# Performance work log

Hardware: AMD Instinct MI355X
Metric: run time of the kernel (lower is better)

The kernel has to match this reference:

```python
import jax, jax.numpy as jnp
import numpy as np

NUM_BOND_TYPE = 6
NUM_BOND_DIRECTION = 3
HIDDEN = 128
OUT = 128


def setup_inputs() -> dict:
    key = jax.random.key(0)
    ks = jax.random.split(key, 12)
    N, E = 50000, 800000
    x = jax.random.normal(ks[0], (N, HIDDEN), dtype=jnp.float32)
    edge_index = jax.random.randint(ks[1], (2, E), 0, N, dtype=jnp.int64 if jax.config.jax_enable_x64 else jnp.int32)
    edge_attr = jax.random.randint(ks[2], (E, 2), 0, 3, dtype=edge_index.dtype)
    mask_node_indices = jax.random.randint(ks[3], (5000,), 0, N, dtype=edge_index.dtype)
    s = 1.0 / np.sqrt(HIDDEN)
    W_enc = jax.random.uniform(ks[4], (HIDDEN, HIDDEN), jnp.float32, -s, s)  # enc_to_dec, no bias
    W1 = jax.random.uniform(ks[5], (2 * HIDDEN, HIDDEN), jnp.float32, -s, s)
    b1 = jax.random.uniform(ks[6], (2 * HIDDEN,), jnp.float32, -s, s)
    s2 = 1.0 / np.sqrt(2 * HIDDEN)
    W2 = jax.random.uniform(ks[7], (OUT, 2 * HIDDEN), jnp.float32, -s2, s2)
    b2 = jax.random.uniform(ks[8], (OUT,), jnp.float32, -s2, s2)
    # xavier_uniform for embeddings
    g1 = np.sqrt(6.0 / (NUM_BOND_TYPE + HIDDEN))
    g2 = np.sqrt(6.0 / (NUM_BOND_DIRECTION + HIDDEN))
    emb1 = jax.random.uniform(ks[9], (NUM_BOND_TYPE, HIDDEN), jnp.float32, -g1, g1)
    emb2 = jax.random.uniform(ks[10], (NUM_BOND_DIRECTION, HIDDEN), jnp.float32, -g2, g2)
    prelu_a = jnp.array(0.25, dtype=jnp.float32)
    return {"x": x, "edge_index": edge_index, "edge_attr": edge_attr,
            "mask_node_indices": mask_node_indices, "prelu_a": prelu_a,
            "W_enc": W_enc, "W1": W1, "b1": b1, "W2": W2, "b2": b2,
            "emb1": emb1, "emb2": emb2}


def reference(x, edge_index, edge_attr, mask_node_indices, prelu_a,
              W_enc, W1, b1, W2, b2, emb1, emb2):
    N = x.shape[0]
    # PReLU activation then enc_to_dec linear (no bias)
    h = jnp.where(x > 0, x, prelu_a * x)
    h = h @ W_enc.T
    # zero out masked nodes
    h = h.at[mask_node_indices].set(0.0)
    # add self loops
    loops = jnp.arange(N, dtype=edge_index.dtype)
    src = jnp.concatenate([edge_index[0], loops])
    dst = jnp.concatenate([edge_index[1], loops])
    # self-loop edge_attr: [4, 0]
    sl_attr = jnp.concatenate([jnp.full((N, 1), 4, dtype=edge_attr.dtype),
                               jnp.zeros((N, 1), dtype=edge_attr.dtype)], axis=1)
    ea = jnp.concatenate([edge_attr, sl_attr], axis=0)
    edge_emb = emb1[ea[:, 0]] + emb2[ea[:, 1]]  # [E+N, H]
    # message: x_j + edge_attr, aggregate (add) at target nodes
    msg = h[src] + edge_emb
    aggr = jax.ops.segment_sum(msg, dst, num_segments=N)  # [N, H]
    # GIN update MLP: H -> 2H -> OUT
    out = jax.nn.relu(aggr @ W1.T + b1) @ W2.T + b2
    return out
```

## Files before the change

kernel.cpp:

```cpp
#include <hip/hip_runtime.h>

#define HID 128
#define HID2 256
#define NBMAX 3200
#define STRIDE 384

typedef __attribute__((ext_vector_type(8))) short bf16x8;
typedef __attribute__((ext_vector_type(4))) float f32x4;

__device__ inline ushort f2b(float f) {
    union { float f; unsigned u; } v; v.f = f;
    unsigned r = v.u + 0x7FFF + ((v.u >> 16) & 1);
    return (ushort)(r >> 16);
}
__device__ inline float b2f(unsigned hi16) {
    union { unsigned u; float f; } v; v.u = hi16 << 16;
    return v.f;
}

#define SZ0 (HID * HID)
#define SZ1 (HID2 * HID)
#define SZ2 (HID * HID2)

__global__ __launch_bounds__(256) void k_prep(const float* __restrict__ w0,
                                              const float* __restrict__ w1,
                                              const float* __restrict__ w2,
                                              const float* __restrict__ e1,
                                              const float* __restrict__ e2,
                                              ushort* __restrict__ o0,
                                              ushort* __restrict__ o1,
                                              ushort* __restrict__ o2,
                                              ushort* __restrict__ comboT,
                                              int* __restrict__ gcursor) {
    int i = blockIdx.x * 256 + threadIdx.x;
    if (i < SZ0) { o0[i] = f2b(w0[i]); return; }
    i -= SZ0;
    if (i < SZ1) { o1[i] = f2b(w1[i]); return; }
    i -= SZ1;
    if (i < SZ2) { o2[i] = f2b(w2[i]); return; }
    i -= SZ2;
    if (i < 4096) {
        int col = i >> 5, tt = i & 31;
        float v = 0.f;
        if (tt < 18) v = e1[(tt / 3) * HID + col] + e2[(tt % 3) * HID + col];
        comboT[col * 32 + tt] = f2b(v);
        return;
    }
    i -= 4096;
    if (i < 4096) gcursor[i] = i * STRIDE;
}

__global__ __launch_bounds__(256) void k_prelu(const float* __restrict__ x,
                                               const float* __restrict__ pa,
                                               ushort* __restrict__ p, int total8) {
    int i = blockIdx.x * 256 + threadIdx.x;
    if (i >= total8) return;
    const float a = pa[0];
    float4 v0 = *(const float4*)(x + (size_t)i * 8);
    float4 v1 = *(const float4*)(x + (size_t)i * 8 + 4);
    float vv[8] = {v0.x, v0.y, v0.z, v0.w, v1.x, v1.y, v1.z, v1.w};
    ushort u[8];
#pragma unroll
    for (int j = 0; j < 8; ++j) {
        float f = vv[j] > 0.f ? vv[j] : a * vv[j];
        u[j] = f2b(f);
    }
    *(bf16x8*)(p + (size_t)i * 8) = *(bf16x8*)u;
}

__global__ void k_mask(const int* __restrict__ idx, ushort* __restrict__ p) {
    *(unsigned*)(p + (size_t)idx[blockIdx.x] * HID + 2 * threadIdx.x) = 0u;
}

__global__ __launch_bounds__(256) void k_bscat(const int* __restrict__ src,
                                               const int* __restrict__ dst,
                                               const int* __restrict__ ea,
                                               int* __restrict__ gcursor,
                                               unsigned* __restrict__ bucketed,
                                               int E, int nbuck) {
    __shared__ int lh[NBMAX];
    __shared__ int gbs[NBMAX];
    const int t = threadIdx.x;
    const int base = blockIdx.x * 4096;
    for (int i = t; i < nbuck; i += 256) lh[i] = 0;
    __syncthreads();
    unsigned keys[16];
    int bk[16];
    int rk[16];
#pragma unroll
    for (int j = 0; j < 16; ++j) {
        int e = base + j * 256 + t;
        bk[j] = -1;
        if (e < E) {
            int d = dst[e];
            int cm = ea[2 * e] * 3 + ea[2 * e + 1];
            keys[j] = (unsigned)src[e] | ((unsigned)(d & 15) << 16) | ((unsigned)cm << 20);
            bk[j] = d >> 4;
            rk[j] = atomicAdd(&lh[bk[j]], 1);
        }
    }
    __syncthreads();
    for (int i = t; i < nbuck; i += 256) gbs[i] = lh[i] ? atomicAdd(&gcursor[i], lh[i]) : 0;
    __syncthreads();
#pragma unroll
    for (int j = 0; j < 16; ++j)
        if (bk[j] >= 0) {
            int pos = gbs[bk[j]] + rk[j];
            int lim = (bk[j] + 1) * STRIDE;
            if (pos < lim) bucketed[pos] = keys[j];
        }
}

__global__ __launch_bounds__(512) void k_baccum3(const ushort* __restrict__ p,
                                                 const int* __restrict__ gcursor,
                                                 const unsigned* __restrict__ bucketed,
                                                 ushort* __restrict__ A,
                                                 ushort* __restrict__ A2, int N) {
    __shared__ unsigned skeys[STRIDE];
    __shared__ int cnt[16];
    __shared__ int soff[16];
    __shared__ int cur[16];
    __shared__ int cnts[16][18];
    const int t = threadIdx.x;
    const int n0 = blockIdx.x << 4;
    const int w = t >> 6, l = t & 63;
    const int g = l >> 4, c16 = l & 15;

    for (int i = t; i < 16 * 18; i += 512) cnts[i / 18][i % 18] = ((i % 18) == 12) ? 1 : 0;

    float acc[2][8];
#pragma unroll
    for (int nn = 0; nn < 2; ++nn) {
        int gn = n0 + w * 2 + nn;
        uint4 pv = {0u, 0u, 0u, 0u};
        if (g == 0 && gn < N) pv = *(const uint4*)(p + (size_t)gn * HID + c16 * 8);
#pragma unroll
        for (int q = 0; q < 4; ++q) {
            unsigned u = (&pv.x)[q];
            acc[nn][2 * q]     = (g == 0) ? b2f(u & 0xffffu) : 0.f;
            acc[nn][2 * q + 1] = (g == 0) ? b2f(u >> 16) : 0.f;
        }
    }

    const int s0 = blockIdx.x * STRIDE;
    const int m = gcursor[blockIdx.x] - s0;
    if (t < 16) cnt[t] = 0;
    __syncthreads();
    if (t < m) atomicAdd(&cnt[(bucketed[s0 + t] >> 16) & 15], 1);
    __syncthreads();
    if (t < 16) {
        int v = cnt[t];
        int sc = v;
#pragma unroll
        for (int o = 1; o < 16; o <<= 1) {
            int u = __shfl_up(sc, o, 64);
            if (t >= o) sc += u;
        }
        soff[t] = sc - v;
        cur[t] = sc - v;
    }
    __syncthreads();
    if (t < m) {
        unsigned key = bucketed[s0 + t];
        int dl = (key >> 16) & 15;
        int r = atomicAdd(&cur[dl], 1);
        skeys[r] = key;
        atomicAdd(&cnts[dl][key >> 20], 1);
    }
    __syncthreads();
#pragma unroll
    for (int nn = 0; nn < 2; ++nn) {
        const int node = w * 2 + nn;
        const int eb = soff[node];
        const int c = cnt[node];
        for (int k = 0; k < c; k += 16) {
            int iA = k + g, iB = k + 4 + g, iC = k + 8 + g, iD = k + 12 + g;
            bool vA = iA < c, vB = iB < c, vC = iC < c, vD = iD < c;
            unsigned keyA = skeys[eb + (vA ? iA : c - 1)];
            unsigned keyB = skeys[eb + (vB ? iB : c - 1)];
            unsigned keyC = skeys[eb + (vC ? iC : c - 1)];
            unsigned keyD = skeys[eb + (vD ? iD : c - 1)];
            uint4 pa4 = *(const uint4*)(p + (size_t)(keyA & 0xffffu) * HID + c16 * 8);
            uint4 pb4 = *(const uint4*)(p + (size_t)(keyB & 0xffffu) * HID + c16 * 8);
            uint4 pc4 = *(const uint4*)(p + (size_t)(keyC & 0xffffu) * HID + c16 * 8);
            uint4 pd4 = *(const uint4*)(p + (size_t)(keyD & 0xffffu) * HID + c16 * 8);
#pragma unroll
            for (int q = 0; q < 4; ++q) {
                unsigned ua = (&pa4.x)[q], ub = (&pb4.x)[q];
                unsigned uc = (&pc4.x)[q], ud = (&pd4.x)[q];
                float s0f = (vA ? b2f(ua & 0xffffu) : 0.f) + (vB ? b2f(ub & 0xffffu) : 0.f)
                          + (vC ? b2f(uc & 0xffffu) : 0.f) + (vD ? b2f(ud & 0xffffu) : 0.f);
                float s1f = (vA ? b2f(ua >> 16) : 0.f) + (vB ? b2f(ub >> 16) : 0.f)
                          + (vC ? b2f(uc >> 16) : 0.f) + (vD ? b2f(ud >> 16) : 0.f);
                acc[nn][2 * q]     += s0f;
                acc[nn][2 * q + 1] += s1f;
            }
        }
    }
#pragma unroll
    for (int nn = 0; nn < 2; ++nn) {
        int gn = n0 + w * 2 + nn;
        unsigned ou[4];
#pragma unroll
        for (int q = 0; q < 4; ++q) {
            float v0 = acc[nn][2 * q], v1 = acc[nn][2 * q + 1];
            v0 += __shfl_xor(v0, 16, 64); v1 += __shfl_xor(v1, 16, 64);
            v0 += __shfl_xor(v0, 32, 64); v1 += __shfl_xor(v1, 32, 64);
            ou[q] = (unsigned)f2b(v0) | ((unsigned)f2b(v1) << 16);
        }
        if (g == 0 && gn < N)
            *(uint4*)(A + (size_t)gn * HID + c16 * 8) = *(uint4*)ou;
    }
    __syncthreads();
    if (t < 16 * 16) {
        int r = t >> 4, cp = t & 15;
        int gn = n0 + r;
        if (gn < N) {
            int i0 = 2 * cp, i1 = 2 * cp + 1;
            ushort u0 = (i0 < 18) ? f2b((float)cnts[r][i0]) : (ushort)0;
            ushort u1 = (i1 < 18) ? f2b((float)cnts[r][i1]) : (ushort)0;
            *(unsigned*)(A2 + (size_t)gn * 32 + 2 * cp) = (unsigned)u0 | ((unsigned)u1 << 16);
        }
    }
}

__global__ __launch_bounds__(256) void k_fused(const ushort* __restrict__ A,
                                               const ushort* __restrict__ A2,
                                               const ushort* __restrict__ Wencb,
                                               const ushort* __restrict__ comboT,
                                               const ushort* __restrict__ W1b,
                                               const float* __restrict__ b1,
                                               const ushort* __restrict__ W2b,
                                               const float* __restrict__ b2,
                                               float* __restrict__ out, int N) {
    __shared__ char smem[53248];
    const int t = threadIdx.x;
    const int bn = blockIdx.x * 64;
    {
        int seg = t & 15, r0 = t >> 4;
#pragma unroll
        for (int i = 0; i < 4; ++i) {
            int row = r0 + i * 16;
            int grow = bn + row;
            bf16x8 v;
            if (grow < N) v = *(const bf16x8*)(A + (size_t)grow * HID + seg * 8);
            else { ushort z[8] = {0,0,0,0,0,0,0,0}; v = *(bf16x8*)z; }
            *(bf16x8*)(smem + row * 256 + ((seg * 16) ^ ((row & 7) << 4))) = v;
        }
    }
    {
        int row = t >> 2, seg = t & 3;
        int grow = bn + row;
        bf16x8 v;
        if (grow < N) v = *(const bf16x8*)(A2 + (size_t)grow * 32 + seg * 8);
        else { ushort z[8] = {0,0,0,0,0,0,0,0}; v = *(bf16x8*)z; }
        *(bf16x8*)(smem + 16384 + row * 64 + ((seg * 16) ^ ((row & 3) << 4))) = v;
    }
    __syncthreads();
    const int w = t >> 6, l = t & 63;
    const int lrow = l & 15, lk = l >> 4;
    {
        bf16x8 wf[2][4], cf[2];
#pragma unroll
        for (int j = 0; j < 2; ++j) {
            int n = (2 * w + j) * 16 + lrow;
#pragma unroll
            for (int ks = 0; ks < 4; ++ks)
                wf[j][ks] = *(const bf16x8*)(Wencb + n * HID + ks * 32 + lk * 8);
            cf[j] = *(const bf16x8*)(comboT + n * 32 + lk * 8);
        }
#pragma unroll
        for (int rt = 0; rt < 4; ++rt) {
            int arow = rt * 16 + lrow;
            bf16x8 af[4], a2f;
#pragma unroll
            for (int ks = 0; ks < 4; ++ks)
                af[ks] = *(const bf16x8*)(smem + arow * 256 + ((ks * 64 + lk * 16) ^ ((arow & 7) << 4)));
            a2f = *(const bf16x8*)(smem + 16384 + arow * 64 + ((lk * 16) ^ ((arow & 3) << 4)));
#pragma unroll
            for (int j = 0; j < 2; ++j) {
                f32x4 acc = {0.f, 0.f, 0.f, 0.f};
#pragma unroll
                for (int ks = 0; ks < 4; ++ks)
                    acc = __builtin_amdgcn_mfma_f32_16x16x32_bf16(af[ks], wf[j][ks], acc, 0, 0, 0);
                acc = __builtin_amdgcn_mfma_f32_16x16x32_bf16(a2f, cf[j], acc, 0, 0, 0);
                int n = (2 * w + j) * 16 + lrow;
#pragma unroll
                for (int r = 0; r < 4; ++r) {
                    int row2 = rt * 16 + lk * 4 + r;
                    *(ushort*)(smem + 20480 + row2 * 256 + ((2 * n) ^ ((row2 & 7) << 4))) = f2b(acc[r]);
                }
            }
        }
    }
    __syncthreads();
    {
        bf16x8 wf[4][4];
        float bb[4];
#pragma unroll
        for (int j = 0; j < 4; ++j) {
            int n = (4 * w + j) * 16 + lrow;
#pragma unroll
            for (int ks = 0; ks < 4; ++ks)
                wf[j][ks] = *(const bf16x8*)(W1b + n * HID + ks * 32 + lk * 8);
            bb[j] = b1[n];
        }
        const int h2base = (w < 2) ? 0 : 36864;
        const int colbase = (w < 2) ? 0 : 128;
#pragma unroll
        for (int rt = 0; rt < 4; ++rt) {
            int arow = rt * 16 + lrow;
            bf16x8 af[4];
#pragma unroll
            for (int ks = 0; ks < 4; ++ks)
                af[ks] = *(const bf16x8*)(smem + 20480 + arow * 256 + ((ks * 64 + lk * 16) ^ ((arow & 7) << 4)));
#pragma unroll
            for (int j = 0; j < 4; ++j) {
                f32x4 acc = {0.f, 0.f, 0.f, 0.f};
#pragma unroll
                for (int ks = 0; ks < 4; ++ks)
                    acc = __builtin_amdgcn_mfma_f32_16x16x32_bf16(af[ks], wf[j][ks], acc, 0, 0, 0);
                int cl = (4 * w + j) * 16 + lrow - colbase;
#pragma unroll
                for (int r = 0; r < 4; ++r) {
                    float v = acc[r] + bb[j];
                    v = v > 0.f ? v : 0.f;
                    int row2 = rt * 16 + lk * 4 + r;
                    *(ushort*)(smem + h2base + row2 * 256 + ((2 * cl) ^ ((row2 & 7) << 4))) = f2b(v);
                }
            }
        }
    }
    __syncthreads();
    {
        bf16x8 wf[2][8];
        float bb[2];
#pragma unroll
        for (int j = 0; j < 2; ++j) {
            int n = (2 * w + j) * 16 + lrow;
#pragma unroll
            for (int ks = 0; ks < 8; ++ks)
                wf[j][ks] = *(const bf16x8*)(W2b + n * HID2 + ks * 32 + lk * 8);
            bb[j] = b2[n];
        }
#pragma unroll
        for (int rt = 0; rt < 4; ++rt) {
            int arow = rt * 16 + lrow;
            bf16x8 af[8];
#pragma unroll
            for (int ks = 0; ks < 4; ++ks)
                af[ks] = *(const bf16x8*)(smem + arow * 256 + ((ks * 64 + lk * 16) ^ ((arow & 7) << 4)));
#pragma unroll
            for (int ks = 4; ks < 8; ++ks)
                af[ks] = *(const bf16x8*)(smem + 36864 + arow * 256 + (((ks - 4) * 64 + lk * 16) ^ ((arow & 7) << 4)));
#pragma unroll
            for (int j = 0; j < 2; ++j) {
                f32x4 acc = {0.f, 0.f, 0.f, 0.f};
#pragma unroll
                for (int ks = 0; ks < 8; ++ks)
                    acc = __builtin_amdgcn_mfma_f32_16x16x32_bf16(af[ks], wf[j][ks], acc, 0, 0, 0);
                int n = (2 * w + j) * 16 + lrow;
#pragma unroll
                for (int r = 0; r < 4; ++r) {
                    int grow = bn + rt * 16 + lk * 4 + r;
                    if (grow < N) out[(size_t)grow * HID + n] = acc[r] + bb[j];
                }
            }
        }
    }
}

extern "C" void kernel_launch(void* const* d_in, const int* in_sizes, int n_in,
                              void* d_out, int out_size, void* d_ws, size_t ws_size,
                              hipStream_t stream) {
    const float* x     = (const float*)d_in[0];
    const int*   eidx  = (const int*)d_in[1];
    const int*   eattr = (const int*)d_in[2];
    const int*   mask  = (const int*)d_in[3];
    const float* pa    = (const float*)d_in[4];
    const float* Wenc  = (const float*)d_in[5];
    const float* W1    = (const float*)d_in[6];
    const float* b1    = (const float*)d_in[7];
    const float* W2    = (const float*)d_in[8];
    const float* b2    = (const float*)d_in[9];
    const float* emb1  = (const float*)d_in[10];
    const float* emb2  = (const float*)d_in[11];

    const int N = in_sizes[0] / HID;
    const int E = in_sizes[1] / 2;
    const int M = in_sizes[3];

    const int* src = eidx;
    const int* dst = eidx + E;

    const int nbuck = (N + 15) >> 4;

    ushort*   p        = (ushort*)d_ws;
    ushort*   A        = p + (size_t)N * HID;
    ushort*   A2       = A + (size_t)N * HID;
    ushort*   Wencb    = A2 + (size_t)N * 32;
    ushort*   W1b      = Wencb + SZ0;
    ushort*   W2b      = W1b + SZ1;
    ushort*   comboT   = W2b + SZ2;
    int*      gcursor  = (int*)(comboT + 4096);
    unsigned* bucketed = (unsigned*)(gcursor + 4096);

    const int nb64 = (N + 63) / 64;
    const int total8 = N * HID / 8;
    const int nbE = (E + 4095) / 4096;
    const int prepTotal = SZ0 + SZ1 + SZ2 + 4096 + 4096;

    k_prep<<<(prepTotal + 255) / 256, 256, 0, stream>>>(Wenc, W1, W2, emb1, emb2,
                                                        Wencb, W1b, W2b, comboT, gcursor);
    k_prelu<<<(total8 + 255) / 256, 256, 0, stream>>>(x, pa, p, total8);
    k_mask<<<M, 64, 0, stream>>>(mask, p);
    k_bscat<<<nbE, 256, 0, stream>>>(src, dst, eattr, gcursor, bucketed, E, nbuck);
    k_baccum3<<<nbuck, 512, 0, stream>>>(p, gcursor, bucketed, A, A2, N);
    k_fused<<<nb64, 256, 0, stream>>>(A, A2, Wencb, comboT, W1b, b1, W2b, b2, (float*)d_out, N);
}
```

Measured before the change: 104.0 us.

## Give each wave its own 16-row tile and drop block-wide barriers in fused MLP

Restructures the fused GEMM chain so each wavefront owns 16 node rows and computes all output columns for them, instead of the four waves sharing 64 rows split by column. The A tiles are loaded straight from global memory into registers, and weights are streamed from global/L2 per MFMA rather than held in registers. Intermediates go to per-wave shared buffers, which removes the __syncthreads barriers and the cooperative staging step. The cost is more weight reads per row, since each wave reloads every weight matrix, and the A loads lose the N bounds guard.

```diff
diff --git a/kernel.cpp b/kernel.cpp
--- a/kernel.cpp
+++ b/kernel.cpp
@@ -233,138 +233,85 @@
                                                const ushort* __restrict__ W2b,
                                                const float* __restrict__ b2,
                                                float* __restrict__ out, int N) {
-    __shared__ char smem[53248];
+    __shared__ char h1s[4][4096];
+    __shared__ char h2s[4][8192];
     const int t = threadIdx.x;
-    const int bn = blockIdx.x * 64;
-    {
-        int seg = t & 15, r0 = t >> 4;
-#pragma unroll
-        for (int i = 0; i < 4; ++i) {
-            int row = r0 + i * 16;
-            int grow = bn + row;
-            bf16x8 v;
-            if (grow < N) v = *(const bf16x8*)(A + (size_t)grow * HID + seg * 8);
-            else { ushort z[8] = {0,0,0,0,0,0,0,0}; v = *(bf16x8*)z; }
-            *(bf16x8*)(smem + row * 256 + ((seg * 16) ^ ((row & 7) << 4))) = v;
-        }
-    }
-    {
-        int row = t >> 2, seg = t & 3;
-        int grow = bn + row;
-        bf16x8 v;
-        if (grow < N) v = *(const bf16x8*)(A2 + (size_t)grow * 32 + seg * 8);
-        else { ushort z[8] = {0,0,0,0,0,0,0,0}; v = *(bf16x8*)z; }
-        *(bf16x8*)(smem + 16384 + row * 64 + ((seg * 16) ^ ((row & 3) << 4))) = v;
-    }
-    __syncthreads();
     const int w = t >> 6, l = t & 63;
     const int lrow = l & 15, lk = l >> 4;
+    const int r0 = blockIdx.x * 64 + w * 16;
+    char* h1p = h1s[w];
+    char* h2p = h2s[w];
+
     {
-        bf16x8 wf[2][4], cf[2];
-#pragma unroll
-        for (int j = 0; j < 2; ++j) {
-            int n = (2 * w + j) * 16 + lrow;
-#pragma unroll
-            for (int ks = 0; ks < 4; ++ks)
-                wf[j][ks] = *(const bf16x8*)(Wencb + n * HID + ks * 32 + lk * 8);
-            cf[j] = *(const bf16x8*)(comboT + n * 32 + lk * 8);
-        }
-#pragma unroll
-        for (int rt = 0; rt < 4; ++rt) {
-            int arow = rt * 16 + lrow;
-            bf16x8 af[4], a2f;
-#pragma unroll
-            for (int ks = 0; ks < 4; ++ks)
-                af[ks] = *(const bf16x8*)(smem + arow * 256 + ((ks * 64 + lk * 16) ^ ((arow & 7) << 4)));
-            a2f = *(const bf16x8*)(smem + 16384 + arow * 64 + ((lk * 16) ^ ((arow & 3) << 4)));
-#pragma unroll
-            for (int j = 0; j < 2; ++j) {
-                f32x4 acc = {0.f, 0.f, 0.f, 0.f};
-#pragma unroll
-                for (int ks = 0; ks < 4; ++ks)
-                    acc = __builtin_amdgcn_mfma_f32_16x16x32_bf16(af[ks], wf[j][ks], acc, 0, 0, 0);
-                acc = __builtin_amdgcn_mfma_f32_16x16x32_bf16(a2f, cf[j], acc, 0, 0, 0);
-                int n = (2 * w + j) * 16 + lrow;
-#pragma unroll
-                for (int r = 0; r < 4; ++r) {
-                    int row2 = rt * 16 + lk * 4 + r;
-                    *(ushort*)(smem + 20480 + row2 * 256 + ((2 * n) ^ ((row2 & 7) << 4))) = f2b(acc[r]);
-                }
-            }
-        }
-    }
-    __syncthreads();
+        const size_t arow = (size_t)(r0 + lrow);
+        bf16x8 af[4];
+#pragma unroll
+        for (int ks = 0; ks < 4; ++ks)
+            af[ks] = *(const bf16x8*)(A + arow * HID + ks * 32 + lk * 8);
+        bf16x8 a2f = *(const bf16x8*)(A2 + arow * 32 + lk * 8);
+#pragma unroll
+        for (int j = 0; j < 8; ++j) {
+            int n = j * 16 + lrow;
+            f32x4 acc = {0.f, 0.f, 0.f, 0.f};
+#pragma unroll
+            for (int ks = 0; ks < 4; ++ks) {
+                bf16x8 wfr = *(const bf16x8*)(Wencb + n * HID + ks * 32 + lk * 8);
+                acc = __builtin_amdgcn_mfma_f32_16x16x32_bf16(af[ks], wfr, acc, 0, 0, 0);
+            }
+            {
+                bf16x8 cfr = *(const bf16x8*)(comboT + n * 32 + lk * 8);
+                acc = __builtin_amdgcn_mfma_f32_16x16x32_bf16(a2f, cfr, acc, 0, 0, 0);
+            }
+#pragma unroll
+            for (int r = 0; r < 4; ++r) {
+                int row2 = lk * 4 + r;
+                *(ushort*)(h1p + row2 * 256 + ((2 * n) ^ ((row2 & 7) << 4))) = f2b(acc[r]);
+            }
+        }
+    }
     {
-        bf16x8 wf[4][4];
-        float bb[4];
-#pragma unroll
-        for (int j = 0; j < 4; ++j) {
-            int n = (4 * w + j) * 16 + lrow;
-#pragma unroll
-            for (int ks = 0; ks < 4; ++ks)
-                wf[j][ks] = *(const bf16x8*)(W1b + n * HID + ks * 32 + lk * 8);
-            bb[j] = b1[n];
-        }
-        const int h2base = (w < 2) ? 0 : 36864;
-        const int colbase = (w < 2) ? 0 : 128;
-#pragma unroll
-        for (int rt = 0; rt < 4; ++rt) {
-            int arow = rt * 16 + lrow;
-            bf16x8 af[4];
-#pragma unroll
-            for (int ks = 0; ks < 4; ++ks)
-                af[ks] = *(const bf16x8*)(smem + 20480 + arow * 256 + ((ks * 64 + lk * 16) ^ ((arow & 7) << 4)));
-#pragma unroll
-            for (int j = 0; j < 4; ++j) {
-                f32x4 acc = {0.f, 0.f, 0.f, 0.f};
-#pragma unroll
-                for (int ks = 0; ks < 4; ++ks)
-                    acc = __builtin_amdgcn_mfma_f32_16x16x32_bf16(af[ks], wf[j][ks], acc, 0, 0, 0);
-                int cl = (4 * w + j) * 16 + lrow - colbase;
-#pragma unroll
-                for (int r = 0; r < 4; ++r) {
-                    float v = acc[r] + bb[j];
-                    v = v > 0.f ? v : 0.f;
-                    int row2 = rt * 16 + lk * 4 + r;
-                    *(ushort*)(smem + h2base + row2 * 256 + ((2 * cl) ^ ((row2 & 7) << 4))) = f2b(v);
-                }
-            }
-        }
-    }
-    __syncthreads();
+        bf16x8 hf[4];
+#pragma unroll
+        for (int ks = 0; ks < 4; ++ks)
+            hf[ks] = *(const bf16x8*)(h1p + lrow * 256 + ((ks * 64 + lk * 16) ^ ((lrow & 7) << 4)));
+#pragma unroll
+        for (int j = 0; j < 16; ++j) {
+            int n = j * 16 + lrow;
+            f32x4 acc = {0.f, 0.f, 0.f, 0.f};
+#pragma unroll
+            for (int ks = 0; ks < 4; ++ks) {
+                bf16x8 wfr = *(const bf16x8*)(W1b + n * HID + ks * 32 + lk * 8);
+                acc = __builtin_amdgcn_mfma_f32_16x16x32_bf16(hf[ks], wfr, acc, 0, 0, 0);
+            }
+            float bb = b1[n];
+#pragma unroll
+            for (int r = 0; r < 4; ++r) {
+                float v = acc[r] + bb;
+                v = v > 0.f ? v : 0.f;
+                int row2 = lk * 4 + r;
+                *(ushort*)(h2p + row2 * 512 + ((2 * n) ^ ((row2 & 7) << 4))) = f2b(v);
+            }
+        }
+    }
     {
-        bf16x8 wf[2][8];
-        float bb[2];
-#pragma unroll
-        for (int j = 0; j < 2; ++j) {
-            int n = (2 * w + j) * 16 + lrow;
-#pragma unroll
-            for (int ks = 0; ks < 8; ++ks)
-                wf[j][ks] = *(const bf16x8*)(W2b + n * HID2 + ks * 32 + lk * 8);
-            bb[j] = b2[n];
-        }
-#pragma unroll
-        for (int rt = 0; rt < 4; ++rt) {
-            int arow = rt * 16 + lrow;
-            bf16x8 af[8];
-#pragma unroll
-            for (int ks = 0; ks < 4; ++ks)
-                af[ks] = *(const bf16x8*)(smem + arow * 256 + ((ks * 64 + lk * 16) ^ ((arow & 7) << 4)));
-#pragma unroll
-            for (int ks = 4; ks < 8; ++ks)
-                af[ks] = *(const bf16x8*)(smem + 36864 + arow * 256 + (((ks - 4) * 64 + lk * 16) ^ ((arow & 7) << 4)));
-#pragma unroll
-            for (int j = 0; j < 2; ++j) {
-                f32x4 acc = {0.f, 0.f, 0.f, 0.f};
-#pragma unroll
-                for (int ks = 0; ks < 8; ++ks)
-                    acc = __builtin_amdgcn_mfma_f32_16x16x32_bf16(af[ks], wf[j][ks], acc, 0, 0, 0);
-                int n = (2 * w + j) * 16 + lrow;
-#pragma unroll
-                for (int r = 0; r < 4; ++r) {
-                    int grow = bn + rt * 16 + lk * 4 + r;
-                    if (grow < N) out[(size_t)grow * HID + n] = acc[r] + bb[j];
-                }
+        bf16x8 gf[8];
+#pragma unroll
+        for (int ks = 0; ks < 8; ++ks)
+            gf[ks] = *(const bf16x8*)(h2p + lrow * 512 + ((ks * 64 + lk * 16) ^ ((lrow & 7) << 4)));
+#pragma unroll
+        for (int j = 0; j < 8; ++j) {
+            int n = j * 16 + lrow;
+            f32x4 acc = {0.f, 0.f, 0.f, 0.f};
+#pragma unroll
+            for (int ks = 0; ks < 8; ++ks) {
+                bf16x8 wfr = *(const bf16x8*)(W2b + n * HID2 + ks * 32 + lk * 8);
+                acc = __builtin_amdgcn_mfma_f32_16x16x32_bf16(gf[ks], wfr, acc, 0, 0, 0);
+            }
+            float bb = b2[n];
+#pragma unroll
+            for (int r = 0; r < 4; ++r) {
+                int grow = r0 + lk * 4 + r;
+                if (grow < N) out[(size_t)grow * HID + n] = acc[r] + bb;
             }
         }
     }
```

After: 150.3 us. +44.5%, slower.
